# Kernel tuning notes

Measured on AMD Instinct MI355X. Metric: run time of the kernel, lower is better.

Reference implementation:

```python
import jax, jax.numpy as jnp
import numpy as np

TEMPERATURE = 1.0


def setup_inputs() -> dict:
    key = jax.random.key(0)
    k1, k2 = jax.random.split(key)
    emb = jax.random.normal(k1, (4096, 1024), dtype=jnp.float32)
    # L2-normalize: module computes cosine similarity via raw dot products and
    # uses unstabilized exp(), so production embeddings are unit-norm.
    emb = emb / jnp.linalg.norm(emb, axis=-1, keepdims=True)
    labels = jax.random.randint(k2, (4096,), 0, 2, dtype=jnp.int64)
    return {"embeddings": emb, "labels": labels}


def reference(embeddings, labels):
    # sim[i,j] = <e_i, e_j> / temperature, shape [B, B]
    sim = jnp.matmul(embeddings, embeddings.T) / TEMPERATURE
    B = sim.shape[0]
    eye = jnp.eye(B, dtype=bool)

    # denominator_i = sum_{j != i} exp(sim[i,j])  ->  log-domain, stable
    logdenom = jax.nn.logsumexp(jnp.where(eye, -jnp.inf, sim), axis=1)  # [B]

    # per-pair loss: -log(exp(sim[i,p]) / denom_i) = logdenom_i - sim[i,p]
    per_pair = logdenom[:, None] - sim  # [B, B]

    is_normal = labels == 0  # [B]
    # positives for row i: p != i with label(p) == 0
    pos_mask = (~eye) & is_normal[None, :]  # [B, B]
    pos_counts = jnp.sum(pos_mask, axis=1)  # [B]

    row_loss = jnp.sum(jnp.where(pos_mask, per_pair, 0.0), axis=1) / jnp.maximum(
        pos_counts, 1
    )  # mean over positives; rows with no positives contribute 0

    n_normal = jnp.sum(is_normal)
    total = jnp.sum(jnp.where(is_normal, row_loss, 0.0))
    loss = jnp.where(n_normal > 0, total / jnp.maximum(n_normal, 1), 0.0)
    return loss
```

## Files before the change

### kernel.cpp

```cpp
#include <hip/hip_runtime.h>
#include <hip/hip_bf16.h>
#include <math.h>

#define B 4096
#define D 1024

#define BM2 256
#define BK2 64
#define NK2 (D / BK2)
#define NB2 (B / BM2)

typedef float f32x4 __attribute__((ext_vector_type(4)));
typedef short s16x8 __attribute__((ext_vector_type(8)));

__device__ inline void gload_lds16(const void* g, void* l) {
    __builtin_amdgcn_global_load_lds(
        (const __attribute__((address_space(1))) void*)g,
        (__attribute__((address_space(3))) void*)l, 16, 0, 0);
}

__global__ __launch_bounds__(256) void prep_kernel(const float* __restrict__ E,
                                                   unsigned short* __restrict__ Ebf,
                                                   float* __restrict__ denomsum,
                                                   float* __restrict__ lblsum) {
    int idx = blockIdx.x * 256 + threadIdx.x;
    if (blockIdx.x < 16) denomsum[idx] = 0.f;
    else if (blockIdx.x < 32) lblsum[idx - 4096] = 0.f;
    const float4* src = (const float4*)E;
    const int n4 = B * D / 4;
    for (int i = idx; i < n4; i += gridDim.x * 256) {
        float4 v = src[i];
        __hip_bfloat16 b0 = __float2bfloat16(v.x);
        __hip_bfloat16 b1 = __float2bfloat16(v.y);
        __hip_bfloat16 b2 = __float2bfloat16(v.z);
        __hip_bfloat16 b3 = __float2bfloat16(v.w);
        ushort4 o;
        o.x = *reinterpret_cast<unsigned short*>(&b0);
        o.y = *reinterpret_cast<unsigned short*>(&b1);
        o.z = *reinterpret_cast<unsigned short*>(&b2);
        o.w = *reinterpret_cast<unsigned short*>(&b3);
        *reinterpret_cast<ushort4*>(&Ebf[i * 4]) = o;
    }
}

template <int AH, int NIH>
__device__ inline void doQ(f32x4 acc[8][4], const s16x8 aq[4][2], const s16x8 bq[2][2][2]) {
    __builtin_amdgcn_s_setprio(1);
#pragma unroll
    for (int mi = 0; mi < 4; ++mi)
#pragma unroll
        for (int ni = 0; ni < 2; ++ni)
#pragma unroll
            for (int ks = 0; ks < 2; ++ks)
                acc[AH * 4 + mi][NIH * 2 + ni] = __builtin_amdgcn_mfma_f32_16x16x32_bf16(
                    aq[mi][ks], bq[NIH][ni][ks], acc[AH * 4 + mi][NIH * 2 + ni], 0, 0, 0);
    __builtin_amdgcn_s_setprio(0);
}

__global__ __launch_bounds__(512, 2) void simexp8_kernel(const unsigned short* __restrict__ Ebf,
                                                         const int* __restrict__ labels,
                                                         float* __restrict__ denomsum,
                                                         float* __restrict__ lblsum,
                                                         float* __restrict__ selfsim) {
    __shared__ short lds[2][4][128 * 64];
    const int tid = threadIdx.x;
    const int lane = tid & 63;
    const int wave = tid >> 6;
    const int wm = wave >> 2;
    const int wn = wave & 3;
    const int kh = lane >> 4;
    const int lrow = lane & 15;
    const int bi = blockIdx.x >> 4;
    const int bj = blockIdx.x & 15;
    const int rowBase = bi * BM2;
    const int colBase = bj * BM2;

    const short* gbase = (const short*)Ebf;

    auto stage = [&](int kt, int buf, int h) {
        int gr0 = (h < 2 ? rowBase : colBase) + ((h & 1) ? 128 : 0);
#pragma unroll
        for (int q = 0; q < 2; ++q) {
            int i = q * 512 + tid;
            int r = i >> 3;
            int lc = (i & 7) ^ (r & 7);
            const short* g = gbase + (size_t)(gr0 + r) * D + kt * BK2 + lc * 8;
            gload_lds16(g, &lds[buf][h][i * 8]);
        }
    };

    auto ldA = [&](int buf, int ah, s16x8 (&a)[4][2]) {
#pragma unroll
        for (int mi = 0; mi < 4; ++mi)
#pragma unroll
            for (int ks = 0; ks < 2; ++ks) {
                int rh = ah * 64 + mi * 16 + lrow;
                int c = ks * 4 + kh;
                a[mi][ks] = *(const s16x8*)&lds[buf][wm][rh * 64 + ((c ^ (rh & 7)) << 3)];
            }
    };
    auto ldB = [&](int buf, int nih, s16x8 (&bf)[2][2]) {
        int h = 2 + (wn >> 1);
#pragma unroll
        for (int ni = 0; ni < 2; ++ni)
#pragma unroll
            for (int ks = 0; ks < 2; ++ks) {
                int rh = (wn & 1) * 64 + nih * 32 + ni * 16 + lrow;
                int c = ks * 4 + kh;
                bf[ni][ks] = *(const s16x8*)&lds[buf][h][rh * 64 + ((c ^ (rh & 7)) << 3)];
            }
    };

    f32x4 acc[8][4];
#pragma unroll
    for (int i = 0; i < 8; ++i)
#pragma unroll
        for (int j = 0; j < 4; ++j) acc[i][j] = (f32x4)(0.f);

    s16x8 aq[4][2];
    s16x8 bq[2][2][2];

    stage(0, 0, 0);
    stage(0, 0, 1);
    stage(0, 0, 2);
    stage(0, 0, 3);
    stage(1, 1, 2);
    stage(1, 1, 3);
    asm volatile("s_waitcnt vmcnt(4)" ::: "memory");
    __builtin_amdgcn_s_barrier();

    for (int u = 0; u < NK2; ++u) {
        const int bp = u & 1;
        ldA(bp, 0, aq);
        ldB(bp, 0, bq[0]);
        if (u + 1 < NK2) stage(u + 1, bp ^ 1, 0);
        __builtin_amdgcn_s_barrier();
        asm volatile("s_waitcnt lgkmcnt(0)" ::: "memory");
        __builtin_amdgcn_sched_barrier(0);
        doQ<0, 0>(acc, aq, bq);
        __builtin_amdgcn_s_barrier();
        ldB(bp, 1, bq[1]);
        if (u + 1 < NK2) stage(u + 1, bp ^ 1, 1);
        __builtin_amdgcn_s_barrier();
        asm volatile("s_waitcnt lgkmcnt(0)" ::: "memory");
        __builtin_amdgcn_sched_barrier(0);
        doQ<0, 1>(acc, aq, bq);
        __builtin_amdgcn_s_barrier();
        ldA(bp, 1, aq);
        if (u + 2 < NK2) stage(u + 2, bp, 2);
        __builtin_amdgcn_s_barrier();
        asm volatile("s_waitcnt lgkmcnt(0)" ::: "memory");
        __builtin_amdgcn_sched_barrier(0);
        doQ<1, 1>(acc, aq, bq);
        __builtin_amdgcn_s_barrier();
        if (u + 2 < NK2) stage(u + 2, bp, 3);
        doQ<1, 0>(acc, aq, bq);
        if (u + 2 < NK2) {
            asm volatile("s_waitcnt vmcnt(4)" ::: "memory");
        } else if (u + 1 < NK2) {
            asm volatile("s_waitcnt vmcnt(0)" ::: "memory");
        }
        __builtin_amdgcn_s_barrier();
    }

    float lbm[4];
#pragma unroll
    for (int ni = 0; ni < 4; ++ni)
        lbm[ni] = (labels[colBase + wn * 64 + ni * 16 + lrow] == 0) ? 1.f : 0.f;

#pragma unroll
    for (int mi = 0; mi < 8; ++mi) {
        float rs[4] = {0.f, 0.f, 0.f, 0.f};
        float ps[4] = {0.f, 0.f, 0.f, 0.f};
#pragma unroll
        for (int ni = 0; ni < 4; ++ni) {
            int gcol = colBase + wn * 64 + ni * 16 + lrow;
#pragma unroll
            for (int r = 0; r < 4; ++r) {
                int grow = rowBase + wm * 128 + mi * 16 + kh * 4 + r;
                float sv = acc[mi][ni][r];
                float e = __expf(sv);
                if (grow == gcol) {
                    e = 0.f;
                    selfsim[grow] = sv;
                }
                rs[r] += e;
                ps[r] += sv * lbm[ni];
            }
        }
#pragma unroll
        for (int m = 1; m < 16; m <<= 1)
#pragma unroll
            for (int r = 0; r < 4; ++r) {
                rs[r] += __shfl_xor(rs[r], m, 64);
                ps[r] += __shfl_xor(ps[r], m, 64);
            }
        if (lrow == 0) {
#pragma unroll
            for (int r = 0; r < 4; ++r) {
                int grow = rowBase + wm * 128 + mi * 16 + kh * 4 + r;
                atomicAdd(&denomsum[grow], rs[r]);
                atomicAdd(&lblsum[grow], ps[r]);
            }
        }
    }
}

__global__ __launch_bounds__(1024) void finalize_kernel(const int* __restrict__ labels,
                                                        const float* __restrict__ denomsum,
                                                        const float* __restrict__ lblsum,
                                                        const float* __restrict__ selfsim,
                                                        float* __restrict__ out) {
    __shared__ int ncnt[16];
    __shared__ float tsum[16];
    int tid = threadIdx.x;
    int wv = tid >> 6, ln = tid & 63;

    int cnt = 0;
    for (int j = tid; j < B; j += 1024) cnt += (labels[j] == 0) ? 1 : 0;
    for (int m = 32; m; m >>= 1) cnt += __shfl_xor(cnt, m, 64);
    if (ln == 0) ncnt[wv] = cnt;
    __syncthreads();
    int n_normal = 0;
#pragma unroll
    for (int w = 0; w < 16; ++w) n_normal += ncnt[w];

    float local = 0.f;
    for (int i = tid; i < B; i += 1024) {
        if (labels[i] == 0) {
            int cntp = n_normal - 1;
            if (cntp > 0) {
                float possum = lblsum[i] - selfsim[i];
                local += logf(denomsum[i]) - possum / (float)cntp;
            }
        }
    }
    for (int m = 32; m; m >>= 1) local += __shfl_xor(local, m, 64);
    if (ln == 0) tsum[wv] = local;
    __syncthreads();
    if (tid == 0) {
        float t = 0.f;
#pragma unroll
        for (int w = 0; w < 16; ++w) t += tsum[w];
        out[0] = (n_normal > 0) ? t / (float)n_normal : 0.f;
    }
}

extern "C" void kernel_launch(void* const* d_in, const int* in_sizes, int n_in,
                              void* d_out, int out_size, void* d_ws, size_t ws_size,
                              hipStream_t stream) {
    const float* E = (const float*)d_in[0];
    const int* labels = (const int*)d_in[1];
    float* out = (float*)d_out;

    char* ws = (char*)d_ws;
    size_t off = 0;
    unsigned short* Ebf = (unsigned short*)(ws + off);
    off += (size_t)B * D * 2;
    float* denomsum = (float*)(ws + off);
    off += B * sizeof(float);
    float* lblsum = (float*)(ws + off);
    off += B * sizeof(float);
    float* selfsim = (float*)(ws + off);
    off += B * sizeof(float);

    prep_kernel<<<2048, 256, 0, stream>>>(E, Ebf, denomsum, lblsum);
    simexp8_kernel<<<NB2 * NB2, 512, 0, stream>>>(Ebf, labels, denomsum, lblsum, selfsim);
    finalize_kernel<<<1, 1024, 0, stream>>>(labels, denomsum, lblsum, selfsim, out);
}
```

Before: 56.38 us.

## Switch to 32x32x16 bf16 MFMA tiles and XCD-aware block remapping

Replaces the 16x16x32 MFMA fragments with 32x32x16 ones, reshaping the accumulators, the LDS fragment loads and the epilogue row/column mapping to match. Larger MFMA tiles need fewer LDS fragment reads per FLOP and fewer instructions. It also remaps block indices so blocks on the same XCD share row and column panels, aiming for better L2 reuse. The epilogue now does wider shuffle reductions (5 steps over 16 values), which adds instruction cost and register pressure.

```diff
diff --git a/kernel.cpp b/kernel.cpp
--- a/kernel.cpp
+++ b/kernel.cpp
@@ -10,7 +10,7 @@
 #define NK2 (D / BK2)
 #define NB2 (B / BM2)
 
-typedef float f32x4 __attribute__((ext_vector_type(4)));
+typedef float f32x16 __attribute__((ext_vector_type(16)));
 typedef short s16x8 __attribute__((ext_vector_type(8)));
 
 __device__ inline void gload_lds16(const void* g, void* l) {
@@ -44,16 +44,14 @@
 }
 
 template <int AH, int NIH>
-__device__ inline void doQ(f32x4 acc[8][4], const s16x8 aq[4][2], const s16x8 bq[2][2][2]) {
+__device__ inline void doQ(f32x16 acc[4][2], const s16x8 aq[2][4], const s16x8 bq[2][4]) {
     __builtin_amdgcn_s_setprio(1);
 #pragma unroll
-    for (int mi = 0; mi < 4; ++mi)
-#pragma unroll
-        for (int ni = 0; ni < 2; ++ni)
-#pragma unroll
-            for (int ks = 0; ks < 2; ++ks)
-                acc[AH * 4 + mi][NIH * 2 + ni] = __builtin_amdgcn_mfma_f32_16x16x32_bf16(
-                    aq[mi][ks], bq[NIH][ni][ks], acc[AH * 4 + mi][NIH * 2 + ni], 0, 0, 0);
+    for (int ks = 0; ks < 4; ++ks)
+#pragma unroll
+        for (int mi = 0; mi < 2; ++mi)
+            acc[AH * 2 + mi][NIH] = __builtin_amdgcn_mfma_f32_32x32x16_bf16(
+                aq[mi][ks], bq[NIH][ks], acc[AH * 2 + mi][NIH], 0, 0, 0);
     __builtin_amdgcn_s_setprio(0);
 }
 
@@ -68,10 +66,12 @@
     const int wave = tid >> 6;
     const int wm = wave >> 2;
     const int wn = wave & 3;
-    const int kh = lane >> 4;
-    const int lrow = lane & 15;
-    const int bi = blockIdx.x >> 4;
-    const int bj = blockIdx.x & 15;
+    const int l31 = lane & 31;
+    const int kg = lane >> 5;
+    const int xcd = blockIdx.x & 7;
+    const int kk = blockIdx.x >> 3;
+    const int bi = (xcd >> 1) * 4 + (kk & 3);
+    const int bj = (xcd & 1) * 8 + (kk >> 2);
     const int rowBase = bi * BM2;
     const int colBase = bj * BM2;
 
@@ -89,36 +89,34 @@
         }
     };
 
-    auto ldA = [&](int buf, int ah, s16x8 (&a)[4][2]) {
-#pragma unroll
-        for (int mi = 0; mi < 4; ++mi)
-#pragma unroll
-            for (int ks = 0; ks < 2; ++ks) {
-                int rh = ah * 64 + mi * 16 + lrow;
-                int c = ks * 4 + kh;
+    auto ldA = [&](int buf, int ah, s16x8 (&a)[2][4]) {
+#pragma unroll
+        for (int mi = 0; mi < 2; ++mi)
+#pragma unroll
+            for (int ks = 0; ks < 4; ++ks) {
+                int rh = ah * 64 + mi * 32 + l31;
+                int c = ks * 2 + kg;
                 a[mi][ks] = *(const s16x8*)&lds[buf][wm][rh * 64 + ((c ^ (rh & 7)) << 3)];
             }
     };
-    auto ldB = [&](int buf, int nih, s16x8 (&bf)[2][2]) {
+    auto ldB = [&](int buf, int nh, s16x8 (&bf)[4]) {
         int h = 2 + (wn >> 1);
 #pragma unroll
-        for (int ni = 0; ni < 2; ++ni)
-#pragma unroll
-            for (int ks = 0; ks < 2; ++ks) {
-                int rh = (wn & 1) * 64 + nih * 32 + ni * 16 + lrow;
-                int c = ks * 4 + kh;
-                bf[ni][ks] = *(const s16x8*)&lds[buf][h][rh * 64 + ((c ^ (rh & 7)) << 3)];
-            }
+        for (int ks = 0; ks < 4; ++ks) {
+            int rh = (wn & 1) * 64 + nh * 32 + l31;
+            int c = ks * 2 + kg;
+            bf[ks] = *(const s16x8*)&lds[buf][h][rh * 64 + ((c ^ (rh & 7)) << 3)];
+        }
     };
 
-    f32x4 acc[8][4];
-#pragma unroll
-    for (int i = 0; i < 8; ++i)
-#pragma unroll
-        for (int j = 0; j < 4; ++j) acc[i][j] = (f32x4)(0.f);
-
-    s16x8 aq[4][2];
-    s16x8 bq[2][2][2];
+    f32x16 acc[4][2];
+#pragma unroll
+    for (int i = 0; i < 4; ++i)
+#pragma unroll
+        for (int j = 0; j < 2; ++j) acc[i][j] = (f32x16)(0.f);
+
+    s16x8 aq[2][4];
+    s16x8 bq[2][4];
 
     stage(0, 0, 0);
     stage(0, 0, 1);
@@ -163,44 +161,48 @@
         __builtin_amdgcn_s_barrier();
     }
 
-    float lbm[4];
-#pragma unroll
-    for (int ni = 0; ni < 4; ++ni)
-        lbm[ni] = (labels[colBase + wn * 64 + ni * 16 + lrow] == 0) ? 1.f : 0.f;
-
-#pragma unroll
-    for (int mi = 0; mi < 8; ++mi) {
-        float rs[4] = {0.f, 0.f, 0.f, 0.f};
-        float ps[4] = {0.f, 0.f, 0.f, 0.f};
-#pragma unroll
-        for (int ni = 0; ni < 4; ++ni) {
-            int gcol = colBase + wn * 64 + ni * 16 + lrow;
-#pragma unroll
-            for (int r = 0; r < 4; ++r) {
-                int grow = rowBase + wm * 128 + mi * 16 + kh * 4 + r;
-                float sv = acc[mi][ni][r];
+    float lbm[2];
+#pragma unroll
+    for (int ni = 0; ni < 2; ++ni)
+        lbm[ni] = (labels[colBase + wn * 64 + ni * 32 + l31] == 0) ? 1.f : 0.f;
+
+#pragma unroll
+    for (int mi = 0; mi < 4; ++mi) {
+        float rs[16], ps[16];
+#pragma unroll
+        for (int g = 0; g < 16; ++g) {
+            rs[g] = 0.f;
+            ps[g] = 0.f;
+        }
+#pragma unroll
+        for (int ni = 0; ni < 2; ++ni) {
+            int gcol = colBase + wn * 64 + ni * 32 + l31;
+#pragma unroll
+            for (int g = 0; g < 16; ++g) {
+                int grow = rowBase + wm * 128 + mi * 32 + (g & 3) + 8 * (g >> 2) + 4 * kg;
+                float sv = acc[mi][ni][g];
                 float e = __expf(sv);
                 if (grow == gcol) {
                     e = 0.f;
                     selfsim[grow] = sv;
                 }
-                rs[r] += e;
-                ps[r] += sv * lbm[ni];
-            }
-        }
-#pragma unroll
-        for (int m = 1; m < 16; m <<= 1)
-#pragma unroll
-            for (int r = 0; r < 4; ++r) {
-                rs[r] += __shfl_xor(rs[r], m, 64);
-                ps[r] += __shfl_xor(ps[r], m, 64);
-            }
-        if (lrow == 0) {
-#pragma unroll
-            for (int r = 0; r < 4; ++r) {
-                int grow = rowBase + wm * 128 + mi * 16 + kh * 4 + r;
-                atomicAdd(&denomsum[grow], rs[r]);
-                atomicAdd(&lblsum[grow], ps[r]);
+                rs[g] += e;
+                ps[g] += sv * lbm[ni];
+            }
+        }
+#pragma unroll
+        for (int m = 1; m < 32; m <<= 1)
+#pragma unroll
+            for (int g = 0; g < 16; ++g) {
+                rs[g] += __shfl_xor(rs[g], m, 64);
+                ps[g] += __shfl_xor(ps[g], m, 64);
+            }
+        if (l31 == 0) {
+#pragma unroll
+            for (int g = 0; g < 16; ++g) {
+                int grow = rowBase + wm * 128 + mi * 32 + (g & 3) + 8 * (g >> 2) + 4 * kg;
+                atomicAdd(&denomsum[grow], rs[g]);
+                atomicAdd(&lblsum[grow], ps[g]);
             }
         }
     }
```

Measured after the change: 84.79 us. 50.4% more time.

## Switch similarity GEMM from bf16 to fp8 scaled MFMA with 128-wide K tiles

Applied to the files above, without the earlier changes.

The prep kernel now converts embeddings to fp8 (e4m3) instead of bf16, and the similarity GEMM uses the 16x16x128 f8f6f4 scaled MFMA with unit scales. The K tile grows to 128 bytes per row, so the LDS footprint per stage is unchanged while the number of K iterations halves. This halves the GEMM's global and LDS traffic and raises matrix throughput, but it costs precision in the dot products, which then feed exp and logsumexp and may affect loss accuracy.

```diff
diff --git a/kernel.cpp b/kernel.cpp
--- a/kernel.cpp
+++ b/kernel.cpp
@@ -6,12 +6,13 @@
 #define D 1024
 
 #define BM2 256
-#define BK2 64
+#define BK2 128
 #define NK2 (D / BK2)
 #define NB2 (B / BM2)
 
 typedef float f32x4 __attribute__((ext_vector_type(4)));
-typedef short s16x8 __attribute__((ext_vector_type(8)));
+typedef int i32x4 __attribute__((ext_vector_type(4)));
+typedef int i32x8 __attribute__((ext_vector_type(8)));
 
 __device__ inline void gload_lds16(const void* g, void* l) {
     __builtin_amdgcn_global_load_lds(
@@ -20,49 +21,46 @@
 }
 
 __global__ __launch_bounds__(256) void prep_kernel(const float* __restrict__ E,
-                                                   unsigned short* __restrict__ Ebf,
+                                                   unsigned int* __restrict__ E8,
                                                    float* __restrict__ denomsum,
                                                    float* __restrict__ lblsum) {
     int idx = blockIdx.x * 256 + threadIdx.x;
     if (blockIdx.x < 16) denomsum[idx] = 0.f;
     else if (blockIdx.x < 32) lblsum[idx - 4096] = 0.f;
     const float4* src = (const float4*)E;
-    const int n4 = B * D / 4;
-    for (int i = idx; i < n4; i += gridDim.x * 256) {
-        float4 v = src[i];
-        __hip_bfloat16 b0 = __float2bfloat16(v.x);
-        __hip_bfloat16 b1 = __float2bfloat16(v.y);
-        __hip_bfloat16 b2 = __float2bfloat16(v.z);
-        __hip_bfloat16 b3 = __float2bfloat16(v.w);
-        ushort4 o;
-        o.x = *reinterpret_cast<unsigned short*>(&b0);
-        o.y = *reinterpret_cast<unsigned short*>(&b1);
-        o.z = *reinterpret_cast<unsigned short*>(&b2);
-        o.w = *reinterpret_cast<unsigned short*>(&b3);
-        *reinterpret_cast<ushort4*>(&Ebf[i * 4]) = o;
+    const int n8 = B * D / 8;
+    for (int i = idx; i < n8; i += gridDim.x * 256) {
+        float4 v0 = src[i * 2];
+        float4 v1 = src[i * 2 + 1];
+        int lo = __builtin_amdgcn_cvt_pk_fp8_f32(v0.x, v0.y, 0, false);
+        lo = __builtin_amdgcn_cvt_pk_fp8_f32(v0.z, v0.w, lo, true);
+        int hi = __builtin_amdgcn_cvt_pk_fp8_f32(v1.x, v1.y, 0, false);
+        hi = __builtin_amdgcn_cvt_pk_fp8_f32(v1.z, v1.w, hi, true);
+        uint2 o;
+        o.x = (unsigned int)lo;
+        o.y = (unsigned int)hi;
+        *reinterpret_cast<uint2*>(&E8[i * 2]) = o;
     }
 }
 
 template <int AH, int NIH>
-__device__ inline void doQ(f32x4 acc[8][4], const s16x8 aq[4][2], const s16x8 bq[2][2][2]) {
+__device__ inline void doQ(f32x4 acc[8][4], const i32x8 aq[4], const i32x8 bq[2][2]) {
     __builtin_amdgcn_s_setprio(1);
 #pragma unroll
     for (int mi = 0; mi < 4; ++mi)
 #pragma unroll
         for (int ni = 0; ni < 2; ++ni)
-#pragma unroll
-            for (int ks = 0; ks < 2; ++ks)
-                acc[AH * 4 + mi][NIH * 2 + ni] = __builtin_amdgcn_mfma_f32_16x16x32_bf16(
-                    aq[mi][ks], bq[NIH][ni][ks], acc[AH * 4 + mi][NIH * 2 + ni], 0, 0, 0);
+            acc[AH * 4 + mi][NIH * 2 + ni] = __builtin_amdgcn_mfma_scale_f32_16x16x128_f8f6f4(
+                aq[mi], bq[NIH][ni], acc[AH * 4 + mi][NIH * 2 + ni], 0, 0, 0, 127, 0, 127);
     __builtin_amdgcn_s_setprio(0);
 }
 
-__global__ __launch_bounds__(512, 2) void simexp8_kernel(const unsigned short* __restrict__ Ebf,
+__global__ __launch_bounds__(512, 2) void simexp8_kernel(const unsigned char* __restrict__ E8,
                                                          const int* __restrict__ labels,
                                                          float* __restrict__ denomsum,
                                                          float* __restrict__ lblsum,
                                                          float* __restrict__ selfsim) {
-    __shared__ short lds[2][4][128 * 64];
+    __shared__ unsigned char lds[2][4][128 * 128];
     const int tid = threadIdx.x;
     const int lane = tid & 63;
     const int wave = tid >> 6;
@@ -75,8 +73,6 @@
     const int rowBase = bi * BM2;
     const int colBase = bj * BM2;
 
-    const short* gbase = (const short*)Ebf;
-
     auto stage = [&](int kt, int buf, int h) {
         int gr0 = (h < 2 ? rowBase : colBase) + ((h & 1) ? 128 : 0);
 #pragma unroll
@@ -84,31 +80,31 @@
             int i = q * 512 + tid;
             int r = i >> 3;
             int lc = (i & 7) ^ (r & 7);
-            const short* g = gbase + (size_t)(gr0 + r) * D + kt * BK2 + lc * 8;
-            gload_lds16(g, &lds[buf][h][i * 8]);
+            const unsigned char* g = E8 + (size_t)(gr0 + r) * D + kt * BK2 + lc * 16;
+            gload_lds16(g, &lds[buf][h][i * 16]);
         }
     };
 
-    auto ldA = [&](int buf, int ah, s16x8 (&a)[4][2]) {
-#pragma unroll
-        for (int mi = 0; mi < 4; ++mi)
-#pragma unroll
-            for (int ks = 0; ks < 2; ++ks) {
-                int rh = ah * 64 + mi * 16 + lrow;
-                int c = ks * 4 + kh;
-                a[mi][ks] = *(const s16x8*)&lds[buf][wm][rh * 64 + ((c ^ (rh & 7)) << 3)];
-            }
+    auto ldA = [&](int buf, int ah, i32x8 (&a)[4]) {
+#pragma unroll
+        for (int mi = 0; mi < 4; ++mi) {
+            int rh = ah * 64 + mi * 16 + lrow;
+            const unsigned char* base = &lds[buf][wm][rh * 128];
+            i32x4 lo = *(const i32x4*)&base[((2 * kh) ^ (rh & 7)) << 4];
+            i32x4 hi = *(const i32x4*)&base[((2 * kh + 1) ^ (rh & 7)) << 4];
+            a[mi] = __builtin_shufflevector(lo, hi, 0, 1, 2, 3, 4, 5, 6, 7);
+        }
     };
-    auto ldB = [&](int buf, int nih, s16x8 (&bf)[2][2]) {
+    auto ldB = [&](int buf, int nih, i32x8 (&bf)[2]) {
         int h = 2 + (wn >> 1);
 #pragma unroll
-        for (int ni = 0; ni < 2; ++ni)
-#pragma unroll
-            for (int ks = 0; ks < 2; ++ks) {
-                int rh = (wn & 1) * 64 + nih * 32 + ni * 16 + lrow;
-                int c = ks * 4 + kh;
-                bf[ni][ks] = *(const s16x8*)&lds[buf][h][rh * 64 + ((c ^ (rh & 7)) << 3)];
-            }
+        for (int ni = 0; ni < 2; ++ni) {
+            int rh = (wn & 1) * 64 + nih * 32 + ni * 16 + lrow;
+            const unsigned char* base = &lds[buf][h][rh * 128];
+            i32x4 lo = *(const i32x4*)&base[((2 * kh) ^ (rh & 7)) << 4];
+            i32x4 hi = *(const i32x4*)&base[((2 * kh + 1) ^ (rh & 7)) << 4];
+            bf[ni] = __builtin_shufflevector(lo, hi, 0, 1, 2, 3, 4, 5, 6, 7);
+        }
     };
 
     f32x4 acc[8][4];
@@ -117,8 +113,8 @@
 #pragma unroll
         for (int j = 0; j < 4; ++j) acc[i][j] = (f32x4)(0.f);
 
-    s16x8 aq[4][2];
-    s16x8 bq[2][2][2];
+    i32x8 aq[4];
+    i32x8 bq[2][2];
 
     stage(0, 0, 0);
     stage(0, 0, 1);
@@ -255,8 +251,8 @@
 
     char* ws = (char*)d_ws;
     size_t off = 0;
-    unsigned short* Ebf = (unsigned short*)(ws + off);
-    off += (size_t)B * D * 2;
+    unsigned char* E8 = (unsigned char*)(ws + off);
+    off += (size_t)B * D;
     float* denomsum = (float*)(ws + off);
     off += B * sizeof(float);
     float* lblsum = (float*)(ws + off);
@@ -264,7 +260,7 @@
     float* selfsim = (float*)(ws + off);
     off += B * sizeof(float);
 
-    prep_kernel<<<2048, 256, 0, stream>>>(E, Ebf, denomsum, lblsum);
-    simexp8_kernel<<<NB2 * NB2, 512, 0, stream>>>(Ebf, labels, denomsum, lblsum, selfsim);
+    prep_kernel<<<2048, 256, 0, stream>>>(E, (unsigned int*)E8, denomsum, lblsum);
+    simexp8_kernel<<<NB2 * NB2, 512, 0, stream>>>(E8, labels, denomsum, lblsum, selfsim);
     finalize_kernel<<<1, 1024, 0, stream>>>(labels, denomsum, lblsum, selfsim, out);
 }
```

Result: slower. 203.7 us (+261.3%).
